# Kernel tuning notes

Measured on AMD Instinct MI355X. Metric: run time of the kernel, lower is better.

Reference implementation:

```python
import jax, jax.numpy as jnp
import numpy as np

N = 50000      # nodes
E = 600000     # edges
F_IN = 128     # num_features
H = 128        # hidden_dim

def setup_inputs() -> dict:
    key = jax.random.key(0)
    k1, k2, k3 = jax.random.split(key, 3)
    x = jax.random.normal(k1, (N, F_IN), dtype=jnp.float32)
    W = jax.random.normal(k2, (F_IN, H), dtype=jnp.float32) * 0.05
    b = jnp.zeros((H,), dtype=jnp.float32)
    edge_index = jax.random.randint(k3, (2, E), 0, N, dtype=jnp.int64)
    return {"x": x, "W": W, "b": b, "edge_index": edge_index}

def reference(x, W, b, edge_index):
    # GCNConv (PyG default): add self-loops, symmetric deg^-1/2 normalization,
    # out[t] = sum_{(s,t) in E'} norm(s,t) * (x @ W)[s] + b, then relu.
    n = x.shape[0]
    loops = jnp.arange(n, dtype=edge_index.dtype)
    src = jnp.concatenate([edge_index[0], loops])  # [E+N]
    dst = jnp.concatenate([edge_index[1], loops])  # [E+N]
    xw = x @ W                                      # [N, H]
    deg = jax.ops.segment_sum(jnp.ones_like(dst, dtype=xw.dtype), dst,
                              num_segments=n)       # [N], >=1 due to self-loops
    dinv = jax.lax.rsqrt(deg)
    norm = dinv[src] * dinv[dst]                    # [E+N]
    msg = xw[src] * norm[:, None]                   # [E+N, H] gather
    agg = jax.ops.segment_sum(msg, dst, num_segments=n)  # [N, H] scatter-add
    out = jax.nn.relu(agg + b)
    # F.dropout(training=False) is identity in eval mode.
    return out
```

## Files before the change

### kernel.cpp

```cpp
#include <hip/hip_runtime.h>
#include <stdint.h>


#define FDIM 128
#define HDIM 128
#define SCAN_CHUNK 1024

using s8v   = __attribute__((ext_vector_type(8))) short;
using f32x4 = __attribute__((ext_vector_type(4))) float;

__device__ __forceinline__ unsigned bf16rn(float f) {
    unsigned u = __float_as_uint(f);
    return (u + 0x7fffu + ((u >> 16) & 1u)) >> 16;
}
__device__ __forceinline__ void upfma(unsigned w, float ds, float& lo, float& hi) {
    lo = fmaf(ds, __uint_as_float(w << 16), lo);
    hi = fmaf(ds, __uint_as_float(w & 0xffff0000u), hi);
}

__global__ __launch_bounds__(256) void k_setup(int* __restrict__ deg,
                                               const float* __restrict__ W,
                                               uint4* __restrict__ Warr,
                                               int n, int packW) {
    const int i = blockIdx.x * 256 + threadIdx.x;
    if (i < n) deg[i] = 0;
    if (packW && i < (FDIM / 8) * HDIM) {
        const int chunk = i >> 7, nn = i & 127;
        float v[8];
#pragma unroll
        for (int j = 0; j < 8; ++j) v[j] = W[(chunk * 8 + j) * HDIM + nn];
        uint4 o;
        o.x = bf16rn(v[0]) | (bf16rn(v[1]) << 16);
        o.y = bf16rn(v[2]) | (bf16rn(v[3]) << 16);
        o.z = bf16rn(v[4]) | (bf16rn(v[5]) << 16);
        o.w = bf16rn(v[6]) | (bf16rn(v[7]) << 16);
        Warr[i] = o;
    }
}

__global__ __launch_bounds__(256) void k_count_xcast(const int* __restrict__ dst,
                                                     int* __restrict__ deg,
                                                     int* __restrict__ slot,
                                                     const float* __restrict__ x,
                                                     uint4* __restrict__ xb,
                                                     int e, int n, int fillBlocks) {
    if ((int)blockIdx.x < fillBlocks) {
        const int i = blockIdx.x * 256 + threadIdx.x;
        if (i < e) slot[i] = atomicAdd(&deg[dst[i]], 1);
    } else if (xb) {
        const long long idx = (long long)(blockIdx.x - fillBlocks) * 256 + threadIdx.x;
        if (idx >= (long long)n * (FDIM / 8)) return;
        const float4* xp = (const float4*)x + idx * 2;
        const float4 a = xp[0], b = xp[1];
        uint4 o;
        o.x = bf16rn(a.x) | (bf16rn(a.y) << 16);
        o.y = bf16rn(a.z) | (bf16rn(a.w) << 16);
        o.z = bf16rn(b.x) | (bf16rn(b.y) << 16);
        o.w = bf16rn(b.z) | (bf16rn(b.w) << 16);
        xb[idx] = o;
    }
}

__global__ __launch_bounds__(256) void k_scan1(const int* __restrict__ deg,
                                               int* __restrict__ rowptr,
                                               int* __restrict__ partials,
                                               float* __restrict__ dinv, int n) {
    __shared__ int sdata[256];
    const int tid = threadIdx.x;
    const int base = blockIdx.x * SCAN_CHUNK + tid * 4;
    int v[4];
    int s = 0;
#pragma unroll
    for (int j = 0; j < 4; ++j) {
        int idx = base + j;
        v[j] = (idx < n) ? deg[idx] : 0;
        if (idx < n) dinv[idx] = rsqrtf((float)v[j] + 1.0f);
        s += v[j];
    }
    sdata[tid] = s;
    __syncthreads();
    for (int off = 1; off < 256; off <<= 1) {
        int t = (tid >= off) ? sdata[tid - off] : 0;
        __syncthreads();
        sdata[tid] += t;
        __syncthreads();
    }
    int run = sdata[tid] - s;
#pragma unroll
    for (int j = 0; j < 4; ++j) {
        int idx = base + j;
        if (idx < n) rowptr[idx] = run;
        run += v[j];
    }
    if (tid == 255) {
        partials[blockIdx.x] = sdata[255];
        if (blockIdx.x == (int)gridDim.x - 1) rowptr[n] = sdata[255];
    }
}

__global__ __launch_bounds__(64) void k_scan2(int* __restrict__ partials, int nb) {
    int l = threadIdx.x;
    int v = (l < nb) ? partials[l] : 0;
    int inc = v;
    for (int off = 1; off < 64; off <<= 1) {
        int t = __shfl_up(inc, off);
        if (l >= off) inc += t;
    }
    if (l < nb) partials[l] = inc - v;
}

__global__ __launch_bounds__(256) void k_fill(const int* __restrict__ src,
                                              const int* __restrict__ dst,
                                              const int* __restrict__ slot,
                                              const int* __restrict__ rowptr,
                                              const int* __restrict__ coff,
                                              int* __restrict__ elist, int e) {
    int i = blockIdx.x * 256 + threadIdx.x;
    if (i < e) {
        const int d = dst[i];
        elist[rowptr[d] + coff[d >> 10] + slot[i]] = src[i];
    }
}

__global__ __launch_bounds__(256) void k_gather_gemm(
    const uint4* __restrict__ xb, const float* __restrict__ dinv,
    const int* __restrict__ rowptr, const int* __restrict__ coff,
    const int* __restrict__ elist, const uint4* __restrict__ Warr,
    const float* __restrict__ bias, float* __restrict__ out, int n) {
    __shared__ uint4 zlds[16][16];
    const int tid = threadIdx.x;
    const int r = tid >> 4, q = tid & 15;
    const int node = blockIdx.x * 16 + r;
    const int wave = tid >> 6, lane = tid & 63;
    const int l16 = lane & 15, lg = lane >> 4;

    int beg = 0, end = 0;
    float di = 0.0f;
    if (node < n) {
        beg = rowptr[node] + coff[node >> 10];
        end = rowptr[node + 1] + coff[(node + 1) >> 10];
        di = dinv[node];
    }

    s8v wf[2][4];
#pragma unroll
    for (int ntl = 0; ntl < 2; ++ntl)
#pragma unroll
        for (int ks = 0; ks < 4; ++ks)
            wf[ntl][ks] = *(const s8v*)&Warr[(ks * 4 + lg) * 128 +
                                             (wave * 2 + ntl) * 16 + l16];
    const float bv0 = bias[(wave * 2 + 0) * 16 + l16];
    const float bv1 = bias[(wave * 2 + 1) * 16 + l16];

    if (node < n) {
        const uint4* xq = xb + q;
        float a0 = 0.f, a1 = 0.f, a2 = 0.f, a3 = 0.f,
              a4 = 0.f, a5 = 0.f, a6 = 0.f, a7 = 0.f;
        {
            const uint4 v = xq[(size_t)node * 16];
            upfma(v.x, di, a0, a1); upfma(v.y, di, a2, a3);
            upfma(v.z, di, a4, a5); upfma(v.w, di, a6, a7);
        }
        if (beg < end) {
            const int last = end - 1;
            int sidx[4];
#pragma unroll
            for (int k = 0; k < 4; ++k) {
                const int jj = beg + k;
                sidx[k] = elist[jj < end ? jj : last];
            }
            for (int j = beg; j < end; j += 4) {
                int snext[4];
#pragma unroll
                for (int k = 0; k < 4; ++k) {
                    const int jj = j + 4 + k;
                    snext[k] = elist[jj < end ? jj : last];
                }
                float dw[4];
                uint4 u[4];
#pragma unroll
                for (int k = 0; k < 4; ++k) {
                    dw[k] = (j + k < end) ? dinv[sidx[k]] : 0.0f;
                    u[k] = xq[(size_t)sidx[k] * 16];
                }
#pragma unroll
                for (int k = 0; k < 4; ++k) {
                    upfma(u[k].x, dw[k], a0, a1); upfma(u[k].y, dw[k], a2, a3);
                    upfma(u[k].z, dw[k], a4, a5); upfma(u[k].w, dw[k], a6, a7);
                }
#pragma unroll
                for (int k = 0; k < 4; ++k) sidx[k] = snext[k];
            }
        }
        uint4 o;
        o.x = bf16rn(a0 * di) | (bf16rn(a1 * di) << 16);
        o.y = bf16rn(a2 * di) | (bf16rn(a3 * di) << 16);
        o.z = bf16rn(a4 * di) | (bf16rn(a5 * di) << 16);
        o.w = bf16rn(a6 * di) | (bf16rn(a7 * di) << 16);
        zlds[r][q ^ r] = o;
    }
    __syncthreads();

    s8v afr[4];
#pragma unroll
    for (int ks = 0; ks < 4; ++ks)
        afr[ks] = *(const s8v*)&zlds[l16][(ks * 4 + lg) ^ l16];

#pragma unroll
    for (int ntl = 0; ntl < 2; ++ntl) {
        f32x4 acc = (f32x4){0.f, 0.f, 0.f, 0.f};
#pragma unroll
        for (int ks = 0; ks < 4; ++ks)
            acc = __builtin_amdgcn_mfma_f32_16x16x32_bf16(afr[ks], wf[ntl][ks], acc, 0, 0, 0);
        const int col = (wave * 2 + ntl) * 16 + l16;
        const float bv = ntl ? bv1 : bv0;
#pragma unroll
        for (int rr = 0; rr < 4; ++rr) {
            const int row = blockIdx.x * 16 + lg * 4 + rr;
            if (row < n)
                __builtin_nontemporal_store(fmaxf(acc[rr] + bv, 0.0f),
                                            &out[(size_t)row * HDIM + col]);
        }
    }
}

__global__ __launch_bounds__(256) void k_gather_f32(const float* __restrict__ x,
                                                    const float* __restrict__ dinv,
                                                    const int* __restrict__ rowptr,
                                                    const int* __restrict__ coff,
                                                    const int* __restrict__ elist,
                                                    float* __restrict__ z, int n) {
    const int lane = threadIdx.x & 31;
    const int node = blockIdx.x * 8 + (threadIdx.x >> 5);
    if (node >= n) return;
    const float di = dinv[node];
    float4 v = ((const float4*)(x + (size_t)node * FDIM))[lane];
    float4 sum;
    sum.x = di * v.x; sum.y = di * v.y; sum.z = di * v.z; sum.w = di * v.w;
    const int beg = rowptr[node] + coff[node >> 10];
    const int end = rowptr[node + 1] + coff[(node + 1) >> 10];
    for (int j = beg; j < end; ++j) {
        const int s = elist[j];
        const float ds = dinv[s];
        const float4 u = ((const float4*)(x + (size_t)s * FDIM))[lane];
        sum.x = fmaf(ds, u.x, sum.x);
        sum.y = fmaf(ds, u.y, sum.y);
        sum.z = fmaf(ds, u.z, sum.z);
        sum.w = fmaf(ds, u.w, sum.w);
    }
    float4 o;
    o.x = di * sum.x; o.y = di * sum.y; o.z = di * sum.z; o.w = di * sum.w;
    ((float4*)(z + (size_t)node * FDIM))[lane] = o;
}

__global__ __launch_bounds__(512) void k_gemm_relu(const float* __restrict__ W,
                                                   const float* __restrict__ bias,
                                                   float* __restrict__ zo, int n) {
    __shared__ float Wl[FDIM * HDIM];
    __shared__ float xs[4][FDIM];
    const int t = threadIdx.x;
    const int h = t & (HDIM - 1);
    const int g = t >> 7;
    {
        const float4* W4 = (const float4*)W;
        float4* Wl4 = (float4*)Wl;
        for (int i = t; i < FDIM * HDIM / 4; i += 512) Wl4[i] = W4[i];
    }
    __syncthreads();
    const float bv = bias[h];
    const int nq = (n + 3) >> 2;
    for (int q = blockIdx.x; q < nq; q += gridDim.x) {
        const int row = q * 4 + g;
        if (row < n) xs[g][h] = zo[(size_t)row * HDIM + h];
        __syncthreads();
        if (row < n) {
            float acc = bv;
#pragma unroll
            for (int k = 0; k < FDIM; ++k)
                acc = fmaf(xs[g][k], Wl[k * HDIM + h], acc);
            zo[(size_t)row * HDIM + h] = fmaxf(acc, 0.0f);
        }
        __syncthreads();
    }
}

extern "C" void kernel_launch(void* const* d_in, const int* in_sizes, int n_in,
                              void* d_out, int out_size, void* d_ws, size_t ws_size,
                              hipStream_t stream) {
    const float* x = (const float*)d_in[0];
    const float* W = (const float*)d_in[1];
    const float* b = (const float*)d_in[2];
    const int* ei = (const int*)d_in[3];
    float* out = (float*)d_out;

    const int H = in_sizes[2];
    const int F = in_sizes[1] / H;
    const int N = in_sizes[0] / F;
    const int E = in_sizes[3] / 2;
    const int* srcp = ei;
    const int* dstp = ei + E;

    auto align256 = [](size_t v) { return (v + 255) & ~(size_t)255; };
    char* ws = (char*)d_ws;
    size_t off = 0;
    int* deg = (int*)(ws + off);      off += align256((size_t)N * 4);
    float* dinv = (float*)(ws + off); off += align256((size_t)N * 4);
    int* rowptr = (int*)(ws + off);   off += align256((size_t)(N + 1) * 4);
    int* slot = (int*)(ws + off);     off += align256((size_t)E * 4);
    int* partials = (int*)(ws + off); off += 256;
    int* elist = (int*)(ws + off);    off += align256((size_t)E * 4);
    uint4* xb = (uint4*)(ws + off);   off += align256((size_t)N * FDIM * 2);
    uint4* Warr = (uint4*)(ws + off); off += align256((size_t)(FDIM / 8) * HDIM * 16);
    const bool fast = (ws_size >= off);

    const int nblk_scan = (N + SCAN_CHUNK - 1) / SCAN_CHUNK;
    const int fillBlocks = (E + 255) / 256;

    k_setup<<<(N + 255) / 256, 256, 0, stream>>>(deg, W, fast ? Warr : nullptr,
                                                 N, fast ? 1 : 0);
    if (fast) {
        const long long nchunks = (long long)N * (FDIM / 8);
        const int castBlocks = (int)((nchunks + 255) / 256);
        k_count_xcast<<<fillBlocks + castBlocks, 256, 0, stream>>>(
            dstp, deg, slot, x, xb, E, N, fillBlocks);
    } else {
        k_count_xcast<<<fillBlocks, 256, 0, stream>>>(dstp, deg, slot, x, nullptr,
                                                      E, N, fillBlocks);
    }
    k_scan1<<<nblk_scan, 256, 0, stream>>>(deg, rowptr, partials, dinv, N);
    k_scan2<<<1, 64, 0, stream>>>(partials, nblk_scan);
    k_fill<<<fillBlocks, 256, 0, stream>>>(srcp, dstp, slot, rowptr, partials, elist, E);
    if (fast) {
        k_gather_gemm<<<(N + 15) / 16, 256, 0, stream>>>(xb, dinv, rowptr, partials,
                                                         elist, Warr, b, out, N);
    } else {
        k_gather_f32<<<(N + 7) / 8, 256, 0, stream>>>(x, dinv, rowptr, partials,
                                                      elist, out, N);
        k_gemm_relu<<<512, 512, 0, stream>>>(W, b, out, N);
    }
}
```

Before: 84.95 us.

## Fold block-offset scan into consumers and deepen gather prefetch pipeline

Removes the separate single-block scan2 launch by having each block of k_fill and k_gather_gemm recompute the exclusive scan of the per-chunk partials into shared memory. The gather loop is restructured into a two-stage software pipeline that issues feature-row and dinv loads one group ahead, with edge indices prefetched two groups ahead. W fragment and bias loads move after the gather so fewer registers stay live during it. In exchange every block repeats a small wave scan and a barrier, the fast path is limited to N ≤ 64 chunks, and the extra in-flight loads raise register pressure.

```diff
diff --git a/kernel.cpp b/kernel.cpp
--- a/kernel.cpp
+++ b/kernel.cpp
@@ -113,46 +113,56 @@
                                               const int* __restrict__ dst,
                                               const int* __restrict__ slot,
                                               const int* __restrict__ rowptr,
-                                              const int* __restrict__ coff,
-                                              int* __restrict__ elist, int e) {
-    int i = blockIdx.x * 256 + threadIdx.x;
+                                              const int* __restrict__ partials,
+                                              int* __restrict__ elist, int e, int nb) {
+    __shared__ int coffs[64];
+    const int tid = threadIdx.x;
+    if (tid < 64) {
+        int v = (tid < nb) ? partials[tid] : 0;
+        int inc = v;
+        for (int off = 1; off < 64; off <<= 1) {
+            int t = __shfl_up(inc, off);
+            if (tid >= off) inc += t;
+        }
+        coffs[tid] = inc - v;
+    }
+    __syncthreads();
+    const int i = blockIdx.x * 256 + tid;
     if (i < e) {
         const int d = dst[i];
-        elist[rowptr[d] + coff[d >> 10] + slot[i]] = src[i];
+        elist[rowptr[d] + coffs[d >> 10] + slot[i]] = src[i];
     }
 }
 
 __global__ __launch_bounds__(256) void k_gather_gemm(
     const uint4* __restrict__ xb, const float* __restrict__ dinv,
-    const int* __restrict__ rowptr, const int* __restrict__ coff,
+    const int* __restrict__ rowptr, const int* __restrict__ partials,
     const int* __restrict__ elist, const uint4* __restrict__ Warr,
-    const float* __restrict__ bias, float* __restrict__ out, int n) {
+    const float* __restrict__ bias, float* __restrict__ out, int n, int nb) {
     __shared__ uint4 zlds[16][16];
+    __shared__ int coffs[64];
     const int tid = threadIdx.x;
     const int r = tid >> 4, q = tid & 15;
     const int node = blockIdx.x * 16 + r;
     const int wave = tid >> 6, lane = tid & 63;
     const int l16 = lane & 15, lg = lane >> 4;
 
-    int beg = 0, end = 0;
-    float di = 0.0f;
+    if (tid < 64) {
+        int v = (tid < nb) ? partials[tid] : 0;
+        int inc = v;
+        for (int off = 1; off < 64; off <<= 1) {
+            int t = __shfl_up(inc, off);
+            if (tid >= off) inc += t;
+        }
+        coffs[tid] = inc - v;
+    }
+    __syncthreads();
+
     if (node < n) {
-        beg = rowptr[node] + coff[node >> 10];
-        end = rowptr[node + 1] + coff[(node + 1) >> 10];
-        di = dinv[node];
-    }
-
-    s8v wf[2][4];
-#pragma unroll
-    for (int ntl = 0; ntl < 2; ++ntl)
-#pragma unroll
-        for (int ks = 0; ks < 4; ++ks)
-            wf[ntl][ks] = *(const s8v*)&Warr[(ks * 4 + lg) * 128 +
-                                             (wave * 2 + ntl) * 16 + l16];
-    const float bv0 = bias[(wave * 2 + 0) * 16 + l16];
-    const float bv1 = bias[(wave * 2 + 1) * 16 + l16];
-
-    if (node < n) {
+        const int beg = rowptr[node] + coffs[node >> 10];
+        const int end = rowptr[node + 1] + coffs[(node + 1) >> 10];
+        const float di = dinv[node];
+
         const uint4* xq = xb + q;
         float a0 = 0.f, a1 = 0.f, a2 = 0.f, a3 = 0.f,
               a4 = 0.f, a5 = 0.f, a6 = 0.f, a7 = 0.f;
@@ -163,33 +173,50 @@
         }
         if (beg < end) {
             const int last = end - 1;
-            int sidx[4];
+            float dA[4];
+            uint4 uA[4];
+            int sB[4];
+            {
+                int sA[4];
+#pragma unroll
+                for (int k = 0; k < 4; ++k) {
+                    const int jj = beg + k;
+                    sA[k] = elist[jj < end ? jj : last];
+                }
+#pragma unroll
+                for (int k = 0; k < 4; ++k) {
+                    dA[k] = (beg + k < end) ? dinv[sA[k]] : 0.0f;
+                    uA[k] = xq[(size_t)sA[k] * 16];
+                }
+            }
 #pragma unroll
             for (int k = 0; k < 4; ++k) {
-                const int jj = beg + k;
-                sidx[k] = elist[jj < end ? jj : last];
+                const int jj = beg + 4 + k;
+                sB[k] = elist[jj < end ? jj : last];
             }
             for (int j = beg; j < end; j += 4) {
-                int snext[4];
-#pragma unroll
-                for (int k = 0; k < 4; ++k) {
-                    const int jj = j + 4 + k;
-                    snext[k] = elist[jj < end ? jj : last];
-                }
-                float dw[4];
-                uint4 u[4];
-#pragma unroll
-                for (int k = 0; k < 4; ++k) {
-                    dw[k] = (j + k < end) ? dinv[sidx[k]] : 0.0f;
-                    u[k] = xq[(size_t)sidx[k] * 16];
-                }
-#pragma unroll
-                for (int k = 0; k < 4; ++k) {
-                    upfma(u[k].x, dw[k], a0, a1); upfma(u[k].y, dw[k], a2, a3);
-                    upfma(u[k].z, dw[k], a4, a5); upfma(u[k].w, dw[k], a6, a7);
-                }
-#pragma unroll
-                for (int k = 0; k < 4; ++k) sidx[k] = snext[k];
+                float dB[4];
+                uint4 uB[4];
+#pragma unroll
+                for (int k = 0; k < 4; ++k) {
+                    dB[k] = (j + 4 + k < end) ? dinv[sB[k]] : 0.0f;
+                    uB[k] = xq[(size_t)sB[k] * 16];
+                }
+                int sC[4];
+#pragma unroll
+                for (int k = 0; k < 4; ++k) {
+                    const int jj = j + 8 + k;
+                    sC[k] = elist[jj < end ? jj : last];
+                }
+#pragma unroll
+                for (int k = 0; k < 4; ++k) {
+                    upfma(uA[k].x, dA[k], a0, a1); upfma(uA[k].y, dA[k], a2, a3);
+                    upfma(uA[k].z, dA[k], a4, a5); upfma(uA[k].w, dA[k], a6, a7);
+                }
+#pragma unroll
+                for (int k = 0; k < 4; ++k) {
+                    uA[k] = uB[k]; dA[k] = dB[k]; sB[k] = sC[k];
+                }
             }
         }
         uint4 o;
@@ -201,6 +228,16 @@
     }
     __syncthreads();
 
+    s8v wf[2][4];
+#pragma unroll
+    for (int ntl = 0; ntl < 2; ++ntl)
+#pragma unroll
+        for (int ks = 0; ks < 4; ++ks)
+            wf[ntl][ks] = *(const s8v*)&Warr[(ks * 4 + lg) * 128 +
+                                             (wave * 2 + ntl) * 16 + l16];
+    const float bv0 = bias[(wave * 2 + 0) * 16 + l16];
+    const float bv1 = bias[(wave * 2 + 1) * 16 + l16];
+
     s8v afr[4];
 #pragma unroll
     for (int ks = 0; ks < 4; ++ks)
@@ -221,6 +258,19 @@
                 __builtin_nontemporal_store(fmaxf(acc[rr] + bv, 0.0f),
                                             &out[(size_t)row * HDIM + col]);
         }
+    }
+}
+
+__global__ __launch_bounds__(256) void k_fill_fb(const int* __restrict__ src,
+                                                 const int* __restrict__ dst,
+                                                 const int* __restrict__ slot,
+                                                 const int* __restrict__ rowptr,
+                                                 const int* __restrict__ coff,
+                                                 int* __restrict__ elist, int e) {
+    int i = blockIdx.x * 256 + threadIdx.x;
+    if (i < e) {
+        const int d = dst[i];
+        elist[rowptr[d] + coff[d >> 10] + slot[i]] = src[i];
     }
 }
 
@@ -311,7 +361,7 @@
     int* elist = (int*)(ws + off);    off += align256((size_t)E * 4);
     uint4* xb = (uint4*)(ws + off);   off += align256((size_t)N * FDIM * 2);
     uint4* Warr = (uint4*)(ws + off); off += align256((size_t)(FDIM / 8) * HDIM * 16);
-    const bool fast = (ws_size >= off);
+    const bool fast = (ws_size >= off) && (N <= 64 * SCAN_CHUNK);
 
     const int nblk_scan = (N + SCAN_CHUNK - 1) / SCAN_CHUNK;
     const int fillBlocks = (E + 255) / 256;
@@ -323,17 +373,19 @@
         const int castBlocks = (int)((nchunks + 255) / 256);
         k_count_xcast<<<fillBlocks + castBlocks, 256, 0, stream>>>(
             dstp, deg, slot, x, xb, E, N, fillBlocks);
+        k_scan1<<<nblk_scan, 256, 0, stream>>>(deg, rowptr, partials, dinv, N);
+        k_fill<<<fillBlocks, 256, 0, stream>>>(srcp, dstp, slot, rowptr, partials,
+                                               elist, E, nblk_scan);
+        k_gather_gemm<<<(N + 15) / 16, 256, 0, stream>>>(xb, dinv, rowptr, partials,
+                                                         elist, Warr, b, out, N,
+                                                         nblk_scan);
     } else {
         k_count_xcast<<<fillBlocks, 256, 0, stream>>>(dstp, deg, slot, x, nullptr,
                                                       E, N, fillBlocks);
-    }
-    k_scan1<<<nblk_scan, 256, 0, stream>>>(deg, rowptr, partials, dinv, N);
-    k_scan2<<<1, 64, 0, stream>>>(partials, nblk_scan);
-    k_fill<<<fillBlocks, 256, 0, stream>>>(srcp, dstp, slot, rowptr, partials, elist, E);
-    if (fast) {
-        k_gather_gemm<<<(N + 15) / 16, 256, 0, stream>>>(xb, dinv, rowptr, partials,
-                                                         elist, Warr, b, out, N);
-    } else {
+        k_scan1<<<nblk_scan, 256, 0, stream>>>(deg, rowptr, partials, dinv, N);
+        k_scan2<<<1, 64, 0, stream>>>(partials, nblk_scan);
+        k_fill_fb<<<fillBlocks, 256, 0, stream>>>(srcp, dstp, slot, rowptr, partials,
+                                                  elist, E);
         k_gather_f32<<<(N + 7) / 8, 256, 0, stream>>>(x, dinv, rowptr, partials,
                                                       elist, out, N);
         k_gemm_relu<<<512, 512, 0, stream>>>(W, b, out, N);
```

Result: no change. 84.98 us (+0.0%).
